# Kernel optimization log

Measured on AMD Instinct MI355X. Metric: run time of the kernel, lower is better.

Reference implementation:

```python
import jax, jax.numpy as jnp
import numpy as np

D_MODEL = 512
N_HEAD = 8
D_HEAD = D_MODEL // N_HEAD


def setup_inputs() -> dict:
    key = jax.random.key(0)
    ks = jax.random.split(key, 8)
    B, S, T = 4, 512, 32
    src = jax.random.normal(ks[0], (B, S, D_MODEL), dtype=jnp.float32)
    tgt = jax.random.normal(ks[1], (B, S, T, D_MODEL), dtype=jnp.float32)
    tgt_padding_mask = jax.random.bernoulli(ks[2], 0.1, (B, S, T))
    scale = 1.0 / np.sqrt(D_MODEL)
    in_proj_weight = jax.random.uniform(ks[3], (3 * D_MODEL, D_MODEL), dtype=jnp.float32, minval=-scale, maxval=scale)
    in_proj_bias = jnp.zeros((3 * D_MODEL,), dtype=jnp.float32)
    out_proj_weight = jax.random.uniform(ks[4], (D_MODEL, D_MODEL), dtype=jnp.float32, minval=-scale, maxval=scale)
    out_proj_bias = jnp.zeros((D_MODEL,), dtype=jnp.float32)
    return {
        "src": src,
        "tgt": tgt,
        "tgt_padding_mask": tgt_padding_mask,
        "in_proj_weight": in_proj_weight,
        "in_proj_bias": in_proj_bias,
        "out_proj_weight": out_proj_weight,
        "out_proj_bias": out_proj_bias,
    }


def reference(src, tgt, tgt_padding_mask, in_proj_weight, in_proj_bias, out_proj_weight, out_proj_bias):
    # KNN-style cross attention branch (tgt is [B, S, T, D]).
    B, S, _ = src.shape
    T = tgt.shape[-2]
    w_src, w_tgt = in_proj_weight[:D_MODEL], in_proj_weight[D_MODEL:]
    b_src, b_tgt = in_proj_bias[:D_MODEL], in_proj_bias[D_MODEL:]

    q = src @ w_src.T + b_src                      # [B, S, D]
    kv = tgt @ w_tgt.T + b_tgt                     # [B, S, T, 2D]
    k, v = kv[..., :D_MODEL], kv[..., D_MODEL:]

    # mask handling: drop the mask for queries with no valid tgt, zero them later
    attn_invalid = tgt_padding_mask                # [B, S, T]
    mask_no_tgt_valid = jnp.all(attn_invalid, axis=-1)           # [B, S]
    attn_invalid = attn_invalid & ~mask_no_tgt_valid[..., None]

    q = q.reshape(B, S, N_HEAD, D_HEAD)            # [B, S, H, Dh]
    k = k.reshape(B, S, T, N_HEAD, D_HEAD)
    v = v.reshape(B, S, T, N_HEAD, D_HEAD)

    attn = jnp.einsum("bshd,bsthd->bhst", q, k)    # [B, H, S, T]
    attn = jnp.where(attn_invalid[:, None], -jnp.inf, attn)
    attn = jax.nn.softmax(attn / jnp.sqrt(jnp.asarray(D_HEAD, attn.dtype)), axis=-1)

    out = jnp.einsum("bhst,bsthd->bshd", attn, v).reshape(B, S, D_MODEL)
    out = out @ out_proj_weight.T + out_proj_bias
    out = jnp.where(mask_no_tgt_valid[..., None], 0.0, out)
    return out
```

## Files before the change

kernel.cpp:

```cpp
#include <hip/hip_runtime.h>
#include <hip/hip_bf16.h>


typedef __attribute__((ext_vector_type(8))) short frag8;
typedef __attribute__((ext_vector_type(4))) float f32x4;

__device__ __forceinline__ short f2s(float v) {
    return __builtin_bit_cast(short, __float2bfloat16(v));
}
__device__ __forceinline__ float s2f(short x) {
    return __builtin_bit_cast(float, (unsigned)(unsigned short)x << 16);
}
__device__ __forceinline__ void stv(float* p, float v)          { *p = v; }
__device__ __forceinline__ void stv(__hip_bfloat16* p, float v) { *p = __float2bfloat16(v); }

__device__ __forceinline__ void gl_lds16(const __hip_bfloat16* g, __hip_bfloat16* l) {
    __builtin_amdgcn_global_load_lds(
        (const __attribute__((address_space(1))) unsigned int*)g,
        (__attribute__((address_space(3))) unsigned int*)l, 16, 0, 0);
}

__device__ __forceinline__ frag8 cvt8(const float* p) {
    float4 u = *(const float4*)p, v = *(const float4*)(p + 4);
    frag8 o = { f2s(u.x), f2s(u.y), f2s(u.z), f2s(u.w),
                f2s(v.x), f2s(v.y), f2s(v.z), f2s(v.w) };
    return o;
}

template<bool AF32, bool WF32, typename OUTT>
__device__ __forceinline__
void gemm64x(const void* Aop, const void* Wop,
             const float* __restrict__ bias, OUTT* __restrict__ C,
             const int* __restrict__ zmask,
             int N, int K, int tm, int tn, char* smem, int tid)
{
    short* sA = (short*)smem;
    short* sB = sA + 4096;
    int lane = tid & 63, w = tid >> 6;
    int wm = w >> 1, wn = w & 1;
    int m = lane & 15, q = lane >> 4;
    int sw = (m & 7) * 8;
    int trow = tid >> 3;
    int tcb  = ((tid & 7) ^ (trow & 7)) * 8;
    int wbase = (tid & ~63) * 8;

    f32x4 acc[2][2];
#pragma unroll
    for (int i = 0; i < 2; ++i)
#pragma unroll
        for (int j = 0; j < 2; ++j) acc[i][j] = {0.f, 0.f, 0.f, 0.f};

    for (int k0 = 0; k0 < K; k0 += 64) {
        if constexpr (AF32) {
            const float* Af = (const float*)Aop + (size_t)tm * 64 * K;
#pragma unroll
            for (int s = 0; s < 2; ++s)
                *(frag8*)&sA[s * 2048 + tid * 8] =
                    cvt8(Af + (size_t)(s * 32 + trow) * K + k0 + tcb);
        } else {
            const __hip_bfloat16* Ab = (const __hip_bfloat16*)Aop + (size_t)tm * 64 * K;
            gl_lds16(Ab + (size_t)trow * K + k0 + tcb,        (__hip_bfloat16*)&sA[wbase]);
            gl_lds16(Ab + (size_t)(32 + trow) * K + k0 + tcb, (__hip_bfloat16*)&sA[2048 + wbase]);
        }
        if constexpr (WF32) {
            const float* Wf = (const float*)Wop + (size_t)tn * 64 * K;
#pragma unroll
            for (int s = 0; s < 2; ++s)
                *(frag8*)&sB[s * 2048 + tid * 8] =
                    cvt8(Wf + (size_t)(s * 32 + trow) * K + k0 + tcb);
        } else {
            const __hip_bfloat16* Wb = (const __hip_bfloat16*)Wop + (size_t)tn * 64 * K;
            gl_lds16(Wb + (size_t)trow * K + k0 + tcb,        (__hip_bfloat16*)&sB[wbase]);
            gl_lds16(Wb + (size_t)(32 + trow) * K + k0 + tcb, (__hip_bfloat16*)&sB[2048 + wbase]);
        }
        __syncthreads();
#pragma unroll
        for (int ki = 0; ki < 2; ++ki) {
            frag8 af[2], bf2[2];
#pragma unroll
            for (int i = 0; i < 2; ++i)
                af[i] = *(const frag8*)&sA[(wm * 32 + i * 16 + m) * 64 + ((ki * 32 + q * 8) ^ sw)];
#pragma unroll
            for (int j = 0; j < 2; ++j)
                bf2[j] = *(const frag8*)&sB[(wn * 32 + j * 16 + m) * 64 + ((ki * 32 + q * 8) ^ sw)];
#pragma unroll
            for (int i = 0; i < 2; ++i)
#pragma unroll
                for (int j = 0; j < 2; ++j)
                    acc[i][j] = __builtin_amdgcn_mfma_f32_16x16x32_bf16(
                        af[i], bf2[j], acc[i][j], 0, 0, 0);
        }
        __syncthreads();
    }

    int rb = q * 4;
    bool zr[2][4] = {{false,false,false,false},{false,false,false,false}};
    if (zmask) {
#pragma unroll
        for (int i = 0; i < 2; ++i)
#pragma unroll
            for (int t = 0; t < 4; ++t) {
                int row = tm * 64 + wm * 32 + i * 16 + rb + t;
                const uint4* mp = (const uint4*)(zmask + (size_t)row * 32);
                unsigned a = 0xffffffffu;
#pragma unroll
                for (int u = 0; u < 8; ++u) { uint4 v = mp[u]; a &= v.x & v.y & v.z & v.w; }
                zr[i][t] = (a != 0u);
            }
    }
#pragma unroll
    for (int j = 0; j < 2; ++j) {
        int   col = tn * 64 + wn * 32 + j * 16 + m;
        float bv  = bias[col];
#pragma unroll
        for (int i = 0; i < 2; ++i) {
            int row0 = tm * 64 + wm * 32 + i * 16 + rb;
#pragma unroll
            for (int t = 0; t < 4; ++t) {
                float v = acc[i][j][t] + bv;
                if (zr[i][t]) v = 0.f;
                stv(&C[(size_t)(row0 + t) * N + col], v);
            }
        }
    }
}

__global__ __launch_bounds__(256)
void k_q(const float* __restrict__ src, const float* __restrict__ ipw,
         const float* __restrict__ ipb, __hip_bfloat16* __restrict__ q_bf,
         __hip_bfloat16* __restrict__ Tk)
{
    __shared__ __align__(16) char smem[16384];
    int b = blockIdx.x, tid = threadIdx.x;
    gemm64x<true, true, __hip_bfloat16>(src, ipw, ipb, q_bf, nullptr,
                                        512, 512, b >> 3, b & 7, smem, tid);
    if (b < 128) {
        __syncthreads();
        short (*tile)[65] = (short(*)[65])smem;
        int bx = b & 15, by = b >> 4;
        const float* sp = ipw + (size_t)512 * 512;
#pragma unroll
        for (int i = 0; i < 16; ++i) {
            int idx = i * 256 + tid;
            int r = idx >> 6, c = idx & 63;
            tile[r][c] = f2s(sp[(size_t)(bx * 64 + r) * 512 + by * 64 + c]);
        }
        __syncthreads();
        short* Tks = (short*)Tk;
#pragma unroll
        for (int i = 0; i < 16; ++i) {
            int idx = i * 256 + tid;
            int rr = idx >> 6, cc = idx & 63;
            Tks[(size_t)(by * 64 + rr) * 1024 + bx * 64 + cc] = tile[cc][rr];
        }
    }
}

__global__ __launch_bounds__(256)
void k_qk(const __hip_bfloat16* __restrict__ q_bf,
          const __hip_bfloat16* __restrict__ Tk,
          __hip_bfloat16* __restrict__ qkh)
{
    __shared__ short sO[32 * 132];
    int tid = threadIdx.x, wv = tid >> 6, lane = tid & 63;
    int t   = blockIdx.x * 4 + wv;
    int z   = t >> 10, loc = t & 1023;
    int tm  = loc >> 4, tn = loc & 15;
    int r   = lane & 15, kq = (lane >> 4) << 3;

    const __hip_bfloat16* Ap = q_bf + (size_t)z * 64 + (size_t)(tm * 32 + r) * 512 + kq;
    const __hip_bfloat16* Wp = Tk  + (size_t)z * 64 + (size_t)(tn * 32 + r) * 1024 + kq;

    f32x4 acc[2][2];
#pragma unroll
    for (int i = 0; i < 2; ++i)
#pragma unroll
        for (int j = 0; j < 2; ++j) acc[i][j] = {0.f, 0.f, 0.f, 0.f};

#pragma unroll
    for (int k0 = 0; k0 < 64; k0 += 32) {
        frag8 a[2], bb[2];
#pragma unroll
        for (int i = 0; i < 2; ++i) a[i]  = *(const frag8*)(Ap + (size_t)i * 16 * 512 + k0);
#pragma unroll
        for (int j = 0; j < 2; ++j) bb[j] = *(const frag8*)(Wp + (size_t)j * 16 * 1024 + k0);
#pragma unroll
        for (int i = 0; i < 2; ++i)
#pragma unroll
            for (int j = 0; j < 2; ++j)
                acc[i][j] = __builtin_amdgcn_mfma_f32_16x16x32_bf16(a[i], bb[j], acc[i][j], 0, 0, 0);
    }

    int rb = (lane >> 4) * 4;
#pragma unroll
    for (int j = 0; j < 2; ++j)
#pragma unroll
        for (int i = 0; i < 2; ++i)
#pragma unroll
            for (int tq = 0; tq < 4; ++tq)
                sO[(i * 16 + rb + tq) * 132 + wv * 32 + j * 16 + r] = f2s(acc[i][j][tq]);
    __syncthreads();

    int tb  = blockIdx.x * 4;
    int zb  = tb >> 10, locb = tb & 1023;
    int tmb = locb >> 4, tnb = locb & 15;
#pragma unroll
    for (int i = 0; i < 4; ++i) {
        int u = i * 256 + tid;
        int lr = u >> 5, c4 = (u & 31) * 4;
        *(ushort4*)&qkh[(size_t)(tmb * 32 + lr) * 4096 + zb * 512 + tnb * 32 + c4] =
            *(const ushort4*)&sO[lr * 132 + c4];
    }
}

__global__ __launch_bounds__(256)
void k_attn(const float* __restrict__ tgt,
            const __hip_bfloat16* __restrict__ qkh,
            const int* __restrict__ mask,
            __hip_bfloat16* __restrict__ tbar)
{
    int bs   = blockIdx.x;
    int tid  = threadIdx.x;
    int lane = tid & 63;
    int wv   = tid >> 6;
    int m    = lane & 15;
    int g4   = lane >> 4;

    __shared__ short sS[32 * 520];
    __shared__ short sQK[8 * 520];
    __shared__ int   sM[32];

    const float* tg = tgt + (size_t)bs * 32 * 512;
#pragma unroll
    for (int i = 0; i < 16; ++i) {
        int idx = i * 256 + tid;
        int row = idx >> 7, c4 = (idx & 127) * 4;
        float4 v = *(const float4*)(tg + (size_t)row * 512 + c4);
        ushort4 o;
        o.x = (unsigned short)f2s(v.x); o.y = (unsigned short)f2s(v.y);
        o.z = (unsigned short)f2s(v.z); o.w = (unsigned short)f2s(v.w);
        *(ushort4*)&sS[row * 520 + c4] = o;
    }
    const ushort4* qk4 = (const ushort4*)(qkh + (size_t)bs * 4096);
#pragma unroll
    for (int i = 0; i < 4; ++i) {
        int u = i * 256 + tid;
        int h = u >> 7, c4 = (u & 127) * 4;
        *(ushort4*)&sQK[h * 520 + c4] = qk4[u];
    }
    if (tid < 32) sM[tid] = mask[bs * 32 + tid];
    __syncthreads();

    int mk0 = sM[m], mk1 = sM[16 + m];
    bool allm = __all((mk0 != 0) && (mk1 != 0));

    f32x4 acc0 = {0.f,0.f,0.f,0.f}, acc1 = {0.f,0.f,0.f,0.f};
    {
        const short* qb  = &sQK[(m & 7) * 520 + g4 * 8];
        const short* t0p = &sS[m * 520 + g4 * 8];
        const short* t1p = t0p + 16 * 520;
#pragma unroll
        for (int k0 = 0; k0 < 512; k0 += 32) {
            frag8 af = *(const frag8*)(qb + k0);
            frag8 b0 = *(const frag8*)(t0p + k0);
            frag8 b1 = *(const frag8*)(t1p + k0);
            acc0 = __builtin_amdgcn_mfma_f32_16x16x32_bf16(af, b0, acc0, 0, 0, 0);
            acc1 = __builtin_amdgcn_mfma_f32_16x16x32_bf16(af, b1, acc1, 0, 0, 0);
        }
    }

    float p0v[4], p1v[4];
#pragma unroll
    for (int r = 0; r < 4; ++r) {
        float s0 = acc0[r] * 0.125f, s1 = acc1[r] * 0.125f;
        if (!allm) {
            if (mk0) s0 = -__builtin_inff();
            if (mk1) s1 = -__builtin_inff();
        }
        float mx = fmaxf(s0, s1);
#pragma unroll
        for (int off = 1; off < 16; off <<= 1) mx = fmaxf(mx, __shfl_xor(mx, off));
        float e0 = __expf(s0 - mx), e1 = __expf(s1 - mx);
        float sm = e0 + e1;
#pragma unroll
        for (int off = 1; off < 16; off <<= 1) sm += __shfl_xor(sm, off);
        float inv = 1.f / sm;
        p0v[r] = e0 * inv; p1v[r] = e1 * inv;
    }
    __syncthreads();

    short* sPw = sQK + wv * 512;
    if (g4 < 2) {
#pragma unroll
        for (int r = 0; r < 4; ++r) {
            int h = g4 * 4 + r;
            short h0 = f2s(p0v[r]), h1 = f2s(p1v[r]);
            sPw[h * 32 + m]            = h0;
            sPw[h * 32 + 16 + m]       = h1;
            sPw[256 + h * 32 + m]      = f2s(p0v[r] - s2f(h0));
            sPw[256 + h * 32 + 16 + m] = f2s(p1v[r] - s2f(h1));
        }
    }
    __syncthreads();
    frag8 paH = *(const frag8*)(sPw + (m & 7) * 32 + g4 * 8);
    frag8 paL = *(const frag8*)(sPw + 256 + (m & 7) * 32 + g4 * 8);
    __syncthreads();

    short* sO = sQK;
#pragma unroll
    for (int ci = 0; ci < 8; ++ci) {
        int cg = wv * 8 + ci;
        int cbase = cg * 16 + m;
        frag8 vb;
#pragma unroll
        for (int j = 0; j < 8; ++j)
            vb[j] = sS[(g4 * 8 + j) * 520 + cbase];
        f32x4 d = {0.f,0.f,0.f,0.f};
        d = __builtin_amdgcn_mfma_f32_16x16x32_bf16(paH, vb, d, 0, 0, 0);
        d = __builtin_amdgcn_mfma_f32_16x16x32_bf16(paL, vb, d, 0, 0, 0);
        if (g4 < 2) {
#pragma unroll
            for (int r = 0; r < 4; ++r)
                sO[(g4 * 4 + r) * 512 + cg * 16 + m] = f2s(d[r]);
        }
    }
    __syncthreads();

    ushort4* dst = (ushort4*)(tbar + (size_t)bs * 4096);
    const ushort4* so4 = (const ushort4*)sO;
#pragma unroll
    for (int i = 0; i < 4; ++i)
        dst[i * 256 + tid] = so4[i * 256 + tid];
}

__global__ __launch_bounds__(256)
void k_ao(const __hip_bfloat16* __restrict__ tbar, const float* __restrict__ ipw,
          const float* __restrict__ ipb, __hip_bfloat16* __restrict__ ao_bf)
{
    int tid = threadIdx.x, lane = tid & 63;
    int gw = blockIdx.x * 4 + (tid >> 6);
    int z = gw >> 7, loc = gw & 127;
    int tm = loc >> 1, tn = loc & 1;
    int r = lane & 15, kq = (lane >> 4) << 3;

    const __hip_bfloat16* Ap = tbar + (size_t)z * 512 + (size_t)(tm * 32 + r) * 4096 + kq;
    const float*          Wp = ipw + (size_t)(1024 + z * 64 + tn * 32 + r) * 512 + kq;

    f32x4 acc[2][2];
#pragma unroll
    for (int i = 0; i < 2; ++i)
#pragma unroll
        for (int j = 0; j < 2; ++j) acc[i][j] = {0.f, 0.f, 0.f, 0.f};

    for (int k0 = 0; k0 < 512; k0 += 32) {
        frag8 a[2], bb[2];
#pragma unroll
        for (int i = 0; i < 2; ++i) a[i] = *(const frag8*)(Ap + (size_t)i * 16 * 4096 + k0);
#pragma unroll
        for (int j = 0; j < 2; ++j) bb[j] = cvt8(Wp + (size_t)j * 16 * 512 + k0);
#pragma unroll
        for (int i = 0; i < 2; ++i)
#pragma unroll
            for (int j = 0; j < 2; ++j)
                acc[i][j] = __builtin_amdgcn_mfma_f32_16x16x32_bf16(a[i], bb[j], acc[i][j], 0, 0, 0);
    }

    int rb = (lane >> 4) * 4;
#pragma unroll
    for (int j = 0; j < 2; ++j) {
        int   col = tn * 32 + j * 16 + r;
        float bv  = ipb[1024 + z * 64 + col];
#pragma unroll
        for (int i = 0; i < 2; ++i) {
            int row0 = tm * 32 + i * 16 + rb;
#pragma unroll
            for (int t = 0; t < 4; ++t)
                ao_bf[(size_t)(row0 + t) * 512 + z * 64 + col] =
                    __float2bfloat16(acc[i][j][t] + bv);
        }
    }
}

__global__ __launch_bounds__(256)
void k_out(const __hip_bfloat16* __restrict__ ao_bf, const float* __restrict__ opw,
           const float* __restrict__ opb, float* __restrict__ out,
           const int* __restrict__ mask)
{
    __shared__ __align__(16) char smem[16384];
    int b = blockIdx.x;
    gemm64x<false, true, float>(ao_bf, opw, opb, out, mask,
                                512, 512, b >> 3, b & 7, smem, threadIdx.x);
}

extern "C" void kernel_launch(void* const* d_in, const int* in_sizes, int n_in,
                              void* d_out, int out_size, void* d_ws, size_t ws_size,
                              hipStream_t stream)
{
    const float* src  = (const float*)d_in[0];
    const float* tgt  = (const float*)d_in[1];
    const int*   mask = (const int*)d_in[2];
    const float* ipw  = (const float*)d_in[3];
    const float* ipb  = (const float*)d_in[4];
    const float* opw  = (const float*)d_in[5];
    const float* opb  = (const float*)d_in[6];
    float*       out  = (float*)d_out;

    char* ws = (char*)d_ws;
    __hip_bfloat16* q_bf   = (__hip_bfloat16*)(ws + ((size_t)4 << 20));
    __hip_bfloat16* Tk     = (__hip_bfloat16*)(ws + ((size_t)6 << 20));
    __hip_bfloat16* qkh    = (__hip_bfloat16*)(ws + ((size_t)8 << 20));
    __hip_bfloat16* tbar   = (__hip_bfloat16*)(ws + ((size_t)24 << 20));
    __hip_bfloat16* ao_bf  = (__hip_bfloat16*)(ws + ((size_t)40 << 20));

    k_q   <<<256,  256, 0, stream>>>(src, ipw, ipb, q_bf, Tk);
    k_qk  <<<2048, 256, 0, stream>>>(q_bf, Tk, qkh);
    k_attn<<<2048, 256, 0, stream>>>(tgt, qkh, mask, tbar);
    k_ao  <<<256,  256, 0, stream>>>(tbar, ipw, ipb, ao_bf);
    k_out <<<256,  256, 0, stream>>>(ao_bf, opw, opb, out, mask);
}
```

Baseline: 264.0 us.

## Pre-convert weights and src to bf16 in a prep kernel; pad attn LDS rows

Adds a prep kernel that converts in_proj, out_proj and src to bf16 once and builds the transposed K-weight. The GEMMs then use async global-to-LDS loads everywhere instead of converting fp32 inline, and k_ao reads bf16 weights directly. Separately, the tgt tile rows in the attention kernel get extra padding every 8 rows to cut LDS bank conflicts. The cost is one more launch and an extra pass that writes and re-reads the converted buffers.

```diff
diff --git a/kernel.cpp b/kernel.cpp
--- a/kernel.cpp
+++ b/kernel.cpp
@@ -4,6 +4,8 @@
 
 typedef __attribute__((ext_vector_type(8))) short frag8;
 typedef __attribute__((ext_vector_type(4))) float f32x4;
+
+#define SROW(t) ((t) * 520 + ((t) >> 3) * 16)
 
 __device__ __forceinline__ short f2s(float v) {
     return __builtin_bit_cast(short, __float2bfloat16(v));
@@ -20,59 +22,78 @@
         (__attribute__((address_space(3))) unsigned int*)l, 16, 0, 0);
 }
 
-__device__ __forceinline__ frag8 cvt8(const float* p) {
-    float4 u = *(const float4*)p, v = *(const float4*)(p + 4);
-    frag8 o = { f2s(u.x), f2s(u.y), f2s(u.z), f2s(u.w),
-                f2s(v.x), f2s(v.y), f2s(v.z), f2s(v.w) };
-    return o;
-}
-
-template<bool AF32, bool WF32, typename OUTT>
+__global__ __launch_bounds__(256)
+void k_prep(const float* __restrict__ ipw, const float* __restrict__ opw,
+            const float* __restrict__ src,
+            __hip_bfloat16* __restrict__ ipw_bf, __hip_bfloat16* __restrict__ opw_bf,
+            __hip_bfloat16* __restrict__ src_bf, __hip_bfloat16* __restrict__ Tk)
+{
+    __shared__ short tile[64][65];
+    int b = blockIdx.x, tid = threadIdx.x;
+#pragma unroll
+    for (int i = 0; i < 4; ++i) {
+        int g = b * 1024 + i * 256 + tid;
+        const float4* in; ushort4* o4; int off;
+        if (g < 196608)      { in = (const float4*)ipw; o4 = (ushort4*)ipw_bf; off = g; }
+        else if (g < 262144) { in = (const float4*)opw; o4 = (ushort4*)opw_bf; off = g - 196608; }
+        else                 { in = (const float4*)src; o4 = (ushort4*)src_bf; off = g - 262144; }
+        float4 v = in[off];
+        ushort4 o;
+        o.x = (unsigned short)f2s(v.x); o.y = (unsigned short)f2s(v.y);
+        o.z = (unsigned short)f2s(v.z); o.w = (unsigned short)f2s(v.w);
+        o4[off] = o;
+    }
+    if (b < 128) {
+        int bx = b & 15, by = b >> 4;
+        const float* sp = ipw + (size_t)512 * 512;
+#pragma unroll
+        for (int i = 0; i < 16; ++i) {
+            int idx = i * 256 + tid;
+            int r = idx >> 6, c = idx & 63;
+            tile[r][c] = f2s(sp[(size_t)(bx * 64 + r) * 512 + by * 64 + c]);
+        }
+        __syncthreads();
+        short* Tks = (short*)Tk;
+#pragma unroll
+        for (int i = 0; i < 16; ++i) {
+            int idx = i * 256 + tid;
+            int rr = idx >> 6, cc = idx & 63;
+            Tks[(size_t)(by * 64 + rr) * 1024 + bx * 64 + cc] = tile[cc][rr];
+        }
+    }
+}
+
+template<typename OUTT>
 __device__ __forceinline__
-void gemm64x(const void* Aop, const void* Wop,
-             const float* __restrict__ bias, OUTT* __restrict__ C,
-             const int* __restrict__ zmask,
-             int N, int K, int tm, int tn, char* smem, int tid)
+void gemm64_dev(const __hip_bfloat16* __restrict__ A, const __hip_bfloat16* __restrict__ W,
+                const float* __restrict__ bias, OUTT* __restrict__ C,
+                const int* __restrict__ zmask,
+                int N, int K, int tm, int tn, char* smem, int tid)
 {
     short* sA = (short*)smem;
     short* sB = sA + 4096;
     int lane = tid & 63, w = tid >> 6;
     int wm = w >> 1, wn = w & 1;
+    const __hip_bfloat16* Ab = A + (size_t)tm * 64 * K;
+    const __hip_bfloat16* Wb = W + (size_t)tn * 64 * K;
+
+    f32x4 acc[2][2];
+#pragma unroll
+    for (int i = 0; i < 2; ++i)
+#pragma unroll
+        for (int j = 0; j < 2; ++j) acc[i][j] = {0.f, 0.f, 0.f, 0.f};
+
+    int wbase = (tid & ~63) * 8;
     int m = lane & 15, q = lane >> 4;
     int sw = (m & 7) * 8;
     int trow = tid >> 3;
     int tcb  = ((tid & 7) ^ (trow & 7)) * 8;
-    int wbase = (tid & ~63) * 8;
-
-    f32x4 acc[2][2];
-#pragma unroll
-    for (int i = 0; i < 2; ++i)
-#pragma unroll
-        for (int j = 0; j < 2; ++j) acc[i][j] = {0.f, 0.f, 0.f, 0.f};
 
     for (int k0 = 0; k0 < K; k0 += 64) {
-        if constexpr (AF32) {
-            const float* Af = (const float*)Aop + (size_t)tm * 64 * K;
-#pragma unroll
-            for (int s = 0; s < 2; ++s)
-                *(frag8*)&sA[s * 2048 + tid * 8] =
-                    cvt8(Af + (size_t)(s * 32 + trow) * K + k0 + tcb);
-        } else {
-            const __hip_bfloat16* Ab = (const __hip_bfloat16*)Aop + (size_t)tm * 64 * K;
-            gl_lds16(Ab + (size_t)trow * K + k0 + tcb,        (__hip_bfloat16*)&sA[wbase]);
-            gl_lds16(Ab + (size_t)(32 + trow) * K + k0 + tcb, (__hip_bfloat16*)&sA[2048 + wbase]);
-        }
-        if constexpr (WF32) {
-            const float* Wf = (const float*)Wop + (size_t)tn * 64 * K;
-#pragma unroll
-            for (int s = 0; s < 2; ++s)
-                *(frag8*)&sB[s * 2048 + tid * 8] =
-                    cvt8(Wf + (size_t)(s * 32 + trow) * K + k0 + tcb);
-        } else {
-            const __hip_bfloat16* Wb = (const __hip_bfloat16*)Wop + (size_t)tn * 64 * K;
-            gl_lds16(Wb + (size_t)trow * K + k0 + tcb,        (__hip_bfloat16*)&sB[wbase]);
-            gl_lds16(Wb + (size_t)(32 + trow) * K + k0 + tcb, (__hip_bfloat16*)&sB[2048 + wbase]);
-        }
+        gl_lds16(Ab + (size_t)trow * K + k0 + tcb,        (__hip_bfloat16*)&sA[wbase]);
+        gl_lds16(Ab + (size_t)(32 + trow) * K + k0 + tcb, (__hip_bfloat16*)&sA[2048 + wbase]);
+        gl_lds16(Wb + (size_t)trow * K + k0 + tcb,        (__hip_bfloat16*)&sB[wbase]);
+        gl_lds16(Wb + (size_t)(32 + trow) * K + k0 + tcb, (__hip_bfloat16*)&sB[2048 + wbase]);
         __syncthreads();
 #pragma unroll
         for (int ki = 0; ki < 2; ++ki) {
@@ -126,34 +147,13 @@
 }
 
 __global__ __launch_bounds__(256)
-void k_q(const float* __restrict__ src, const float* __restrict__ ipw,
-         const float* __restrict__ ipb, __hip_bfloat16* __restrict__ q_bf,
-         __hip_bfloat16* __restrict__ Tk)
+void k_q(const __hip_bfloat16* src_bf, const __hip_bfloat16* ipw_bf,
+         const float* ipb, __hip_bfloat16* q_bf)
 {
     __shared__ __align__(16) char smem[16384];
-    int b = blockIdx.x, tid = threadIdx.x;
-    gemm64x<true, true, __hip_bfloat16>(src, ipw, ipb, q_bf, nullptr,
-                                        512, 512, b >> 3, b & 7, smem, tid);
-    if (b < 128) {
-        __syncthreads();
-        short (*tile)[65] = (short(*)[65])smem;
-        int bx = b & 15, by = b >> 4;
-        const float* sp = ipw + (size_t)512 * 512;
-#pragma unroll
-        for (int i = 0; i < 16; ++i) {
-            int idx = i * 256 + tid;
-            int r = idx >> 6, c = idx & 63;
-            tile[r][c] = f2s(sp[(size_t)(bx * 64 + r) * 512 + by * 64 + c]);
-        }
-        __syncthreads();
-        short* Tks = (short*)Tk;
-#pragma unroll
-        for (int i = 0; i < 16; ++i) {
-            int idx = i * 256 + tid;
-            int rr = idx >> 6, cc = idx & 63;
-            Tks[(size_t)(by * 64 + rr) * 1024 + bx * 64 + cc] = tile[cc][rr];
-        }
-    }
+    int b = blockIdx.x;
+    gemm64_dev<__hip_bfloat16>(src_bf, ipw_bf, ipb, q_bf, nullptr,
+                               512, 512, b >> 3, b & 7, smem, threadIdx.x);
 }
 
 __global__ __launch_bounds__(256)
@@ -226,7 +226,7 @@
     int m    = lane & 15;
     int g4   = lane >> 4;
 
-    __shared__ short sS[32 * 520];
+    __shared__ short sS[32 * 520 + 64];
     __shared__ short sQK[8 * 520];
     __shared__ int   sM[32];
 
@@ -239,7 +239,7 @@
         ushort4 o;
         o.x = (unsigned short)f2s(v.x); o.y = (unsigned short)f2s(v.y);
         o.z = (unsigned short)f2s(v.z); o.w = (unsigned short)f2s(v.w);
-        *(ushort4*)&sS[row * 520 + c4] = o;
+        *(ushort4*)&sS[SROW(row) + c4] = o;
     }
     const ushort4* qk4 = (const ushort4*)(qkh + (size_t)bs * 4096);
 #pragma unroll
@@ -257,8 +257,8 @@
     f32x4 acc0 = {0.f,0.f,0.f,0.f}, acc1 = {0.f,0.f,0.f,0.f};
     {
         const short* qb  = &sQK[(m & 7) * 520 + g4 * 8];
-        const short* t0p = &sS[m * 520 + g4 * 8];
-        const short* t1p = t0p + 16 * 520;
+        const short* t0p = &sS[SROW(m) + g4 * 8];
+        const short* t1p = &sS[SROW(16 + m) + g4 * 8];
 #pragma unroll
         for (int k0 = 0; k0 < 512; k0 += 32) {
             frag8 af = *(const frag8*)(qb + k0);
@@ -314,7 +314,7 @@
         frag8 vb;
 #pragma unroll
         for (int j = 0; j < 8; ++j)
-            vb[j] = sS[(g4 * 8 + j) * 520 + cbase];
+            vb[j] = sS[SROW(g4 * 8 + j) + cbase];
         f32x4 d = {0.f,0.f,0.f,0.f};
         d = __builtin_amdgcn_mfma_f32_16x16x32_bf16(paH, vb, d, 0, 0, 0);
         d = __builtin_amdgcn_mfma_f32_16x16x32_bf16(paL, vb, d, 0, 0, 0);
@@ -334,7 +334,7 @@
 }
 
 __global__ __launch_bounds__(256)
-void k_ao(const __hip_bfloat16* __restrict__ tbar, const float* __restrict__ ipw,
+void k_ao(const __hip_bfloat16* __restrict__ tbar, const __hip_bfloat16* __restrict__ ipw_bf,
           const float* __restrict__ ipb, __hip_bfloat16* __restrict__ ao_bf)
 {
     int tid = threadIdx.x, lane = tid & 63;
@@ -344,7 +344,7 @@
     int r = lane & 15, kq = (lane >> 4) << 3;
 
     const __hip_bfloat16* Ap = tbar + (size_t)z * 512 + (size_t)(tm * 32 + r) * 4096 + kq;
-    const float*          Wp = ipw + (size_t)(1024 + z * 64 + tn * 32 + r) * 512 + kq;
+    const __hip_bfloat16* Wp = ipw_bf + (size_t)(1024 + z * 64 + tn * 32 + r) * 512 + kq;
 
     f32x4 acc[2][2];
 #pragma unroll
@@ -355,9 +355,9 @@
     for (int k0 = 0; k0 < 512; k0 += 32) {
         frag8 a[2], bb[2];
 #pragma unroll
-        for (int i = 0; i < 2; ++i) a[i] = *(const frag8*)(Ap + (size_t)i * 16 * 4096 + k0);
-#pragma unroll
-        for (int j = 0; j < 2; ++j) bb[j] = cvt8(Wp + (size_t)j * 16 * 512 + k0);
+        for (int i = 0; i < 2; ++i) a[i]  = *(const frag8*)(Ap + (size_t)i * 16 * 4096 + k0);
+#pragma unroll
+        for (int j = 0; j < 2; ++j) bb[j] = *(const frag8*)(Wp + (size_t)j * 16 * 512 + k0);
 #pragma unroll
         for (int i = 0; i < 2; ++i)
 #pragma unroll
@@ -382,14 +382,13 @@
 }
 
 __global__ __launch_bounds__(256)
-void k_out(const __hip_bfloat16* __restrict__ ao_bf, const float* __restrict__ opw,
-           const float* __restrict__ opb, float* __restrict__ out,
-           const int* __restrict__ mask)
+void k_out(const __hip_bfloat16* ao_bf, const __hip_bfloat16* opw_bf,
+           const float* opb, float* out, const int* mask)
 {
     __shared__ __align__(16) char smem[16384];
     int b = blockIdx.x;
-    gemm64x<false, true, float>(ao_bf, opw, opb, out, mask,
-                                512, 512, b >> 3, b & 7, smem, threadIdx.x);
+    gemm64_dev<float>(ao_bf, opw_bf, opb, out, mask,
+                      512, 512, b >> 3, b & 7, smem, threadIdx.x);
 }
 
 extern "C" void kernel_launch(void* const* d_in, const int* in_sizes, int n_in,
@@ -406,15 +405,19 @@
     float*       out  = (float*)d_out;
 
     char* ws = (char*)d_ws;
+    __hip_bfloat16* src_bf = (__hip_bfloat16*)(ws);
+    __hip_bfloat16* ipw_bf = (__hip_bfloat16*)(ws + ((size_t)2 << 20));
+    __hip_bfloat16* opw_bf = (__hip_bfloat16*)(ws + ((size_t)2 << 20) + 1536 * 512 * 2);
     __hip_bfloat16* q_bf   = (__hip_bfloat16*)(ws + ((size_t)4 << 20));
     __hip_bfloat16* Tk     = (__hip_bfloat16*)(ws + ((size_t)6 << 20));
     __hip_bfloat16* qkh    = (__hip_bfloat16*)(ws + ((size_t)8 << 20));
     __hip_bfloat16* tbar   = (__hip_bfloat16*)(ws + ((size_t)24 << 20));
     __hip_bfloat16* ao_bf  = (__hip_bfloat16*)(ws + ((size_t)40 << 20));
 
-    k_q   <<<256,  256, 0, stream>>>(src, ipw, ipb, q_bf, Tk);
+    k_prep<<<512, 256, 0, stream>>>(ipw, opw, src, ipw_bf, opw_bf, src_bf, Tk);
+    k_q   <<<256, 256, 0, stream>>>(src_bf, ipw_bf, ipb, q_bf);
     k_qk  <<<2048, 256, 0, stream>>>(q_bf, Tk, qkh);
     k_attn<<<2048, 256, 0, stream>>>(tgt, qkh, mask, tbar);
-    k_ao  <<<256,  256, 0, stream>>>(tbar, ipw, ipb, ao_bf);
-    k_out <<<256,  256, 0, stream>>>(ao_bf, opw, opb, out, mask);
-}
+    k_ao  <<<256, 256, 0, stream>>>(tbar, ipw_bf, ipb, ao_bf);
+    k_out <<<256, 256, 0, stream>>>(ao_bf, opw_bf, opb, out, mask);
+}
```

Result: faster. 251.8 us (-4.6%).
